# Optimization experiments

Measured on AMD Instinct MI355X. Metric: run time of the kernel, lower is better.

## Reference

```python
import jax, jax.numpy as jnp
import numpy as np
import math

S, B, H, NH = 2048, 2, 2048, 16
HN = H // NH  # 128, head dim


def _rope_cache(seq_len, hn):
    # inv_freqs over even indices, half_hn entries
    inv_freqs = 0.0001 ** (jnp.arange(0, hn, 2, dtype=jnp.float32) / hn)
    pos = jnp.arange(seq_len, dtype=jnp.float32)
    angles = pos[:, None] * inv_freqs  # [s, hn/2]
    return jnp.cos(angles), jnp.sin(angles)


def _apply_rope(x, cos, sin):
    # x: [s, b, np, hn]; cos/sin: [s, hn/2] broadcast over b, np
    half = x.shape[-1] // 2
    c = cos[:, None, None, :]
    s = sin[:, None, None, :]
    left, right = x[..., :half], x[..., half:]
    return jnp.concatenate((c * left - s * right, s * left + c * right), axis=-1)


def setup_inputs() -> dict:
    key = jax.random.key(0)
    k0, k1, k2 = jax.random.split(key, 3)
    hidden_states = jax.random.normal(k0, (S, B, H), dtype=jnp.float32)
    # causal additive mask, broadcast over batch and heads
    causal = jnp.tril(jnp.ones((S, S), dtype=bool))
    attention_mask = jnp.where(causal, 0.0, -1e9).astype(jnp.float32)[None, None]
    W_qkv = jax.random.normal(k1, (3 * H, H), dtype=jnp.float32) * 0.02
    b_qkv = jnp.zeros((3 * H,), dtype=jnp.float32)
    W_dense = jax.random.normal(k2, (H, H), dtype=jnp.float32) * 0.02
    b_dense = jnp.zeros((H,), dtype=jnp.float32)
    return {"hidden_states": hidden_states, "attention_mask": attention_mask,
            "W_qkv": W_qkv, "b_qkv": b_qkv, "W_dense": W_dense, "b_dense": b_dense}


def reference(hidden_states, attention_mask, W_qkv, b_qkv, W_dense, b_dense):
    s, b, h = hidden_states.shape
    # fused QKV projection: [s,b,3h] -> [s,b,np,3*hn] -> split per head
    mixed = hidden_states @ W_qkv.T + b_qkv
    mixed = mixed.reshape(s, b, NH, 3 * HN)
    q, k, v = jnp.split(mixed, 3, axis=-1)  # each [s,b,np,hn]
    cos, sin = _rope_cache(s, HN)
    q = _apply_rope(q, cos, sin)
    k = _apply_rope(k, cos, sin)
    norm_factor = math.sqrt(HN)  # coeff is None (scale_attn_by_inverse_layer_idx=False)
    scores = jnp.einsum('sbnh,tbnh->bnst', q, k) / norm_factor  # [b,np,sq,sk]
    scores = scores + attention_mask
    probs = jax.nn.softmax(scores, axis=-1)  # dropout p=0 in eval
    ctx = jnp.einsum('bnst,tbnh->sbnh', probs, v).reshape(s, b, h)
    return ctx @ W_dense.T + b_dense  # [s,b,h]
```

## Files before the change

kernel.cpp:

```cpp
#include <hip/hip_runtime.h>

#define SEQ   2048
#define BATCH 2
#define HID   2048
#define NHEAD 16
#define HDIM  128
#define MTOT  4096
#define KDIM  2048

typedef __attribute__((ext_vector_type(8))) short  bf16x8;
typedef __attribute__((ext_vector_type(4))) float  f32x4;
typedef __attribute__((ext_vector_type(4))) unsigned short u16x4;
typedef __attribute__((ext_vector_type(8))) unsigned short u16x8;

__device__ __forceinline__ unsigned short f2bf(float x) {
  unsigned u = __float_as_uint(x);
  u += 0x7fffu + ((u >> 16) & 1u);
  return (unsigned short)(u >> 16);
}

__device__ __forceinline__ float fexp2(float x) {
  float r;
  asm("v_exp_f32 %0, %1" : "=v"(r) : "v"(x));
  return r;
}

__device__ __forceinline__ void gl_lds16(const void* g, void* l) {
  __builtin_amdgcn_global_load_lds(
      (__attribute__((address_space(1))) void*)g,
      (__attribute__((address_space(3))) void*)l, 16, 0, 0);
}

__device__ __forceinline__ f32x4 mfma16(bf16x8 a, bf16x8 b, f32x4 c) {
  return __builtin_amdgcn_mfma_f32_16x16x32_bf16(a, b, c, 0, 0, 0);
}

__global__ __launch_bounds__(256, 8)
void conv_swz(const float* __restrict__ src, unsigned short* __restrict__ dst) {
  int i = blockIdx.x * 256 + threadIdx.x;
  int base = i << 2;
  int r = base >> 11, k = base & 2047;
  f32x4 v = *(const f32x4*)(src + base);
  int kp = k ^ (((r >> 1) & 3) << 3);
  u16x4 o;
  o[0] = f2bf(v[0]); o[1] = f2bf(v[1]); o[2] = f2bf(v[2]); o[3] = f2bf(v[3]);
  *(u16x4*)(dst + (size_t)r * 2048 + kp) = o;
}

__global__ __launch_bounds__(256, 8)
void rope_cache_k(float* __restrict__ cosT, float* __restrict__ sinT) {
  int idx = blockIdx.x * 256 + threadIdx.x;
  int s = idx >> 6, i = idx & 63;
  float inv = powf(1e-4f, (float)i * (1.0f / 64.0f));
  float a = (float)s * inv;
  cosT[idx] = cosf(a);
  sinT[idx] = sinf(a);
}

__global__ __launch_bounds__(512, 2)
void gemm_qkv(const unsigned short* __restrict__ A,
              const unsigned short* __restrict__ Bt,
              const float* __restrict__ bias,
              unsigned short* __restrict__ Qs,
              unsigned short* __restrict__ Ks,
              unsigned short* __restrict__ Vp,
              const float* __restrict__ cosT,
              const float* __restrict__ sinT)
{
  __shared__ alignas(16) char lds[98304];
  const int tid = threadIdx.x;
  const int wid = tid >> 6, lane = tid & 63, g = lane >> 4, c = lane & 15;
  const int wr = wid >> 2, wc = wid & 3;

  const int bid = blockIdx.x;
  const int swz = (bid & 7) * 64 + (bid >> 3);
  const int nblk = swz & 15, mblk = swz >> 4;
  const int m0 = mblk << 7;
  const int n0 = nblk * 384;
  const int nh = nblk;

  char* ldsb = (char*)lds;
  const int slotg = (g ^ ((c >> 1) & 3)) << 4;
  const char* ldsAr = ldsb + (wr * 64 + c) * 64 + slotg;
  const char* ldsBr = ldsb + 24576 + (wc * 16 + c) * 64 + slotg;

  const char* gA = (const char*)A  + (size_t)(m0 + (tid >> 2)) * 4096 + (tid & 3) * 16;
  const char* gB = (const char*)Bt + (size_t)(n0 + (tid >> 2)) * 4096 + (tid & 3) * 16;
  char* lA = ldsb + tid * 16;
  char* lB = ldsb + 24576 + tid * 16;

#define STG_A(T, BUF) gl_lds16(gA + (T) * 64, lA + (BUF) * 8192)
#define STG_B(T, BUF) do { const char* _g = gB + (T) * 64; char* _l = lB + (BUF) * 24576; \
    gl_lds16(_g, _l); gl_lds16(_g + 524288, _l + 8192); gl_lds16(_g + 1048576, _l + 16384); } while (0)

  f32x4 acc[4][6];
#pragma unroll
  for (int i = 0; i < 4; ++i)
#pragma unroll
    for (int j = 0; j < 6; ++j) {
      acc[i][j][0] = 0.f; acc[i][j][1] = 0.f; acc[i][j][2] = 0.f; acc[i][j][3] = 0.f;
    }

  bf16x8 a[4], b0[3], b1[3];
  const int NT = KDIM / 32;

#define PH0(BUF, STAGE) do {                                                \
    _Pragma("unroll")                                                       \
    for (int mf = 0; mf < 4; ++mf)                                          \
      a[mf] = *(const bf16x8*)(ldsAr + (BUF) * 8192 + mf * 1024);           \
    _Pragma("unroll")                                                       \
    for (int nl = 0; nl < 3; ++nl)                                          \
      b0[nl] = *(const bf16x8*)(ldsBr + (BUF) * 24576 + nl * 4096);         \
    STAGE;                                                                  \
    __builtin_amdgcn_s_barrier();                                           \
    asm volatile("s_waitcnt lgkmcnt(0)" ::: "memory");                      \
    __builtin_amdgcn_s_setprio(1);                                          \
    _Pragma("unroll")                                                       \
    for (int mf = 0; mf < 4; ++mf)                                          \
      _Pragma("unroll")                                                     \
      for (int nl = 0; nl < 3; ++nl)                                        \
        acc[mf][nl] = mfma16(a[mf], b0[nl], acc[mf][nl]);                   \
    __builtin_amdgcn_s_setprio(0);                                          \
    __builtin_amdgcn_s_barrier();                                           \
  } while (0)

#define PH1(BUF, STAGE, VMW) do {                                           \
    _Pragma("unroll")                                                       \
    for (int nl = 0; nl < 3; ++nl)                                          \
      b1[nl] = *(const bf16x8*)(ldsBr + (BUF) * 24576 + (nl + 3) * 4096);   \
    STAGE;                                                                  \
    __builtin_amdgcn_s_barrier();                                           \
    asm volatile("s_waitcnt lgkmcnt(0)" ::: "memory");                      \
    __builtin_amdgcn_s_setprio(1);                                          \
    _Pragma("unroll")                                                       \
    for (int mf = 0; mf < 4; ++mf)                                          \
      _Pragma("unroll")                                                     \
      for (int nl = 0; nl < 3; ++nl)                                        \
        acc[mf][nl + 3] = mfma16(a[mf], b1[nl], acc[mf][nl + 3]);           \
    __builtin_amdgcn_s_setprio(0);                                          \
    VMW;                                                                    \
    __builtin_amdgcn_s_barrier();                                           \
  } while (0)

#define TILE(T, BUF, BUF2) do {                                             \
    PH0(BUF, { if ((T) + 2 < NT) STG_A((T) + 2, BUF2); });                  \
    PH1(BUF, { if ((T) + 2 < NT) STG_B((T) + 2, BUF2); },                   \
       { if ((T) + 2 < NT) { asm volatile("s_waitcnt vmcnt(4)" ::: "memory"); } \
         else              { asm volatile("s_waitcnt vmcnt(0)" ::: "memory"); } }); \
  } while (0)

  STG_A(0, 0); STG_B(0, 0);
  STG_A(1, 1); STG_B(1, 1);
  asm volatile("s_waitcnt vmcnt(4)" ::: "memory");
  __builtin_amdgcn_s_barrier();

  for (int t = 0; t < 63; t += 3) {
    TILE(t, 0, 2);
    TILE(t + 1, 1, 0);
    TILE(t + 2, 2, 1);
  }
  TILE(63, 0, 2);

  const float qsc = 0.08838834764831845f * 1.4426950408889634f;
  const int dl = wc * 16 + c;
#pragma unroll
  for (int ar = 0; ar < 4; ++ar) {
#pragma unroll
    for (int rr = 0; rr < 4; ++rr) {
      int m = m0 + wr * 64 + ar * 16 + g * 4 + rr;
      int s = m >> 1, bb = m & 1;
      size_t plane = (size_t)(bb * NHEAD + nh) * (SEQ * HDIM);
      int swb = (s & 7) << 3;
      float co = cosT[s * 64 + dl], si = sinT[s * 64 + dl];
      {
        float xl = acc[ar][0][rr] + bias[n0 + dl];
        float xr = acc[ar][1][rr] + bias[n0 + 64 + dl];
        Qs[plane + (size_t)s * HDIM + (dl ^ swb)]        = f2bf((co * xl - si * xr) * qsc);
        Qs[plane + (size_t)s * HDIM + ((dl + 64) ^ swb)] = f2bf((si * xl + co * xr) * qsc);
      }
      {
        float xl = acc[ar][2][rr] + bias[n0 + 128 + dl];
        float xr = acc[ar][3][rr] + bias[n0 + 192 + dl];
        Ks[plane + (size_t)s * HDIM + (dl ^ swb)]        = f2bf(co * xl - si * xr);
        Ks[plane + (size_t)s * HDIM + ((dl + 64) ^ swb)] = f2bf(si * xl + co * xr);
      }
      Vp[plane + (size_t)s * HDIM + dl]      = f2bf(acc[ar][4][rr] + bias[n0 + 256 + dl]);
      Vp[plane + (size_t)s * HDIM + dl + 64] = f2bf(acc[ar][5][rr] + bias[n0 + 320 + dl]);
    }
  }
#undef TILE
#undef PH0
#undef PH1
#undef STG_A
#undef STG_B
}

__global__ __launch_bounds__(512, 2)
void gemm_out(const unsigned short* __restrict__ A,
              const unsigned short* __restrict__ Bt,
              const float* __restrict__ bias,
              float* __restrict__ Cout)
{
  __shared__ alignas(16) char lds[73728];
  const int tid = threadIdx.x;
  const int wid = tid >> 6, lane = tid & 63, g = lane >> 4, c = lane & 15;
  const int wr = wid >> 2, wc = wid & 3;

  const int bid = blockIdx.x;
  const int swz = (bid & 7) * 32 + (bid >> 3);
  const int nblk = swz >> 5, mblk = swz & 31;
  const int m0 = mblk << 7, n0 = nblk << 8;

  char* ldsb = (char*)lds;
  const int slotg = (g ^ ((c >> 1) & 3)) << 4;
  const char* ldsAr = ldsb + (wr * 64 + c) * 64 + slotg;
  const char* ldsBr = ldsb + 24576 + (wc * 64 + c) * 64 + slotg;

  const char* gA = (const char*)A  + (size_t)(m0 + (tid >> 2)) * 4096 + (tid & 3) * 16;
  const char* gB = (const char*)Bt + (size_t)(n0 + (tid >> 2)) * 4096 + (tid & 3) * 16;
  char* lA = ldsb + tid * 16;
  char* lB = ldsb + 24576 + tid * 16;

#define STG_A(T, BUF) gl_lds16(gA + (T) * 64, lA + (BUF) * 8192)
#define STG_B(T, BUF) do { const char* _g = gB + (T) * 64; char* _l = lB + (BUF) * 16384; \
    gl_lds16(_g, _l); gl_lds16(_g + 524288, _l + 8192); } while (0)

  f32x4 acc[4][4];
#pragma unroll
  for (int i = 0; i < 4; ++i)
#pragma unroll
    for (int j = 0; j < 4; ++j) {
      acc[i][j][0] = 0.f; acc[i][j][1] = 0.f; acc[i][j][2] = 0.f; acc[i][j][3] = 0.f;
    }

  bf16x8 a[4], b[4];
  const int NT = KDIM / 32;

#define TILE(T, BUF, BUF2) do {                                             \
    _Pragma("unroll")                                                       \
    for (int mf = 0; mf < 4; ++mf)                                          \
      a[mf] = *(const bf16x8*)(ldsAr + (BUF) * 8192 + mf * 1024);           \
    _Pragma("unroll")                                                       \
    for (int nl = 0; nl < 4; ++nl)                                          \
      b[nl] = *(const bf16x8*)(ldsBr + (BUF) * 16384 + nl * 1024);          \
    if ((T) + 2 < NT) { STG_A((T) + 2, BUF2); STG_B((T) + 2, BUF2); }       \
    __builtin_amdgcn_s_barrier();                                           \
    asm volatile("s_waitcnt lgkmcnt(0)" ::: "memory");                      \
    __builtin_amdgcn_s_setprio(1);                                          \
    _Pragma("unroll")                                                       \
    for (int mf = 0; mf < 4; ++mf)                                          \
      _Pragma("unroll")                                                     \
      for (int nl = 0; nl < 4; ++nl)                                        \
        acc[mf][nl] = mfma16(a[mf], b[nl], acc[mf][nl]);                    \
    __builtin_amdgcn_s_setprio(0);                                          \
    if ((T) + 2 < NT) { asm volatile("s_waitcnt vmcnt(3)" ::: "memory"); }  \
    else              { asm volatile("s_waitcnt vmcnt(0)" ::: "memory"); }  \
    __builtin_amdgcn_s_barrier();                                           \
  } while (0)

  STG_A(0, 0); STG_B(0, 0);
  STG_A(1, 1); STG_B(1, 1);
  asm volatile("s_waitcnt vmcnt(3)" ::: "memory");
  __builtin_amdgcn_s_barrier();

  for (int t = 0; t < 63; t += 3) {
    TILE(t, 0, 2);
    TILE(t + 1, 1, 0);
    TILE(t + 2, 2, 1);
  }
  TILE(63, 0, 2);

#pragma unroll
  for (int mf = 0; mf < 4; ++mf)
#pragma unroll
    for (int rr = 0; rr < 4; ++rr) {
      int m = m0 + wr * 64 + mf * 16 + g * 4 + rr;
#pragma unroll
      for (int nl = 0; nl < 4; ++nl) {
        int n = n0 + wc * 64 + nl * 16 + c;
        Cout[(size_t)m * HID + n] = acc[mf][nl][rr] + bias[n];
      }
    }
#undef TILE
#undef STG_A
#undef STG_B
}

__global__ __launch_bounds__(256, 4)
void transpose_v(const unsigned short* __restrict__ Vp, unsigned short* __restrict__ Vt) {
  __shared__ alignas(16) unsigned short T[64 * 136];
  const int plane = blockIdx.x >> 5;
  const int t0 = (blockIdx.x & 31) << 6;
  const size_t pbase = (size_t)plane * (SEQ * HDIM);
  const int tid = threadIdx.x;
  {
    int t = tid >> 2, d0 = (tid & 3) << 5;
    const unsigned short* src = Vp + pbase + (size_t)(t0 + t) * HDIM + d0;
#pragma unroll
    for (int j = 0; j < 4; ++j) {
      u16x8 v = *(const u16x8*)(src + j * 8);
      *(u16x8*)(&T[t * 136 + d0 + j * 8]) = v;
    }
  }
  __syncthreads();
  {
    int d = tid >> 1, half = tid & 1;
    unsigned short* dstp = Vt + pbase + (size_t)d * SEQ;
    int swb = (d & 7) << 3;
#pragma unroll
    for (int gg = 0; gg < 4; ++gg) {
      u16x8 v;
#pragma unroll
      for (int e = 0; e < 8; ++e)
        v[e] = T[(half * 32 + gg * 8 + e) * 136 + d];
      int tloc = half * 32 + gg * 8;
      *(u16x8*)(dstp + ((t0 + tloc) ^ swb)) = v;
    }
  }
}

__global__ __launch_bounds__(256, 2)
void attn(const unsigned short* __restrict__ Qs,
          const unsigned short* __restrict__ Ks,
          const unsigned short* __restrict__ Vt,
          unsigned short* __restrict__ ctx)
{
  __shared__ alignas(16) unsigned short Klds[2][64 * 128];
  __shared__ alignas(16) unsigned short Vlds[128 * 64];
  __shared__ alignas(16) unsigned short Plds[128 * 72];
  const int tid = threadIdx.x;
  const int w = tid >> 6, lane = tid & 63, g = lane >> 4, c = lane & 15;
  const int bid = blockIdx.x;
  const int head = bid & 31;
  const int qb = (bid < 256) ? (15 - (bid >> 5)) : ((bid >> 5) - 8);
  const int q0 = qb << 7;
  const size_t plane = (size_t)head * (SEQ * HDIM);
  const unsigned short* Qp = Qs + plane;
  const unsigned short* Kp = Ks + plane;
  const unsigned short* Vp = Vt + plane;

  bf16x8 qf[2][4];
#pragma unroll
  for (int q2 = 0; q2 < 2; ++q2) {
    int s = q0 + w * 32 + q2 * 16 + c;
    int swb = (s & 7) << 3;
#pragma unroll
    for (int kk = 0; kk < 4; ++kk) {
      int d0 = kk * 32 + g * 8;
      qf[q2][kk] = *(const bf16x8*)(Qp + (size_t)s * HDIM + (d0 ^ swb));
    }
  }

  f32x4 accO[2][8];
#pragma unroll
  for (int i = 0; i < 2; ++i)
#pragma unroll
    for (int j = 0; j < 8; ++j) {
      accO[i][j][0] = 0.f; accO[i][j][1] = 0.f; accO[i][j][2] = 0.f; accO[i][j][3] = 0.f;
    }
  float mrun[2] = { -1e30f, -1e30f };
  float lrun[2] = { 0.f, 0.f };

  const char* KgBase = (const char*)Kp + (tid >> 4) * 256 + (tid & 15) * 16;
  const char* VgBase = (const char*)Vp + (size_t)(tid >> 3) * 4096 + (tid & 7) * 16;
  char* VldsW = (char*)Vlds + w * 1024;

  const int ntiles = (q0 >> 6) + 2;
  const int qminw = q0 + w * 32;
  const int qmaxw = qminw + 31;

#pragma unroll
  for (int i = 0; i < 4; ++i)
    gl_lds16(KgBase, (char*)Klds[0] + w * 1024 + i * 4096), KgBase += 4096;
  KgBase -= 16384;

  for (int kt = 0; kt < ntiles; ++kt) {
    const int t0 = kt << 6;
    const bool havenext = (kt + 1 < ntiles);

#pragma unroll
    for (int i = 0; i < 4; ++i)
      gl_lds16(VgBase + t0 * 2 + (size_t)i * 131072, VldsW + i * 4096);
    if (havenext) {
      char* kdst = (char*)Klds[(kt + 1) & 1] + w * 1024;
#pragma unroll
      for (int i = 0; i < 4; ++i)
        gl_lds16(KgBase + (size_t)(t0 + 64) * 256 + i * 4096, kdst + i * 4096);
    }
    if (havenext) asm volatile("s_waitcnt vmcnt(8)" ::: "memory");
    else          asm volatile("s_waitcnt vmcnt(4)" ::: "memory");
    __builtin_amdgcn_s_barrier();

    if (t0 <= qmaxw) {
      const char* Kb = (const char*)Klds[kt & 1];
      f32x4 sacc[4][2];
#pragma unroll
      for (int i = 0; i < 4; ++i)
#pragma unroll
        for (int j = 0; j < 2; ++j) {
          sacc[i][j][0] = 0.f; sacc[i][j][1] = 0.f; sacc[i][j][2] = 0.f; sacc[i][j][3] = 0.f;
        }
      __builtin_amdgcn_s_setprio(1);
#pragma unroll
      for (int kk = 0; kk < 4; ++kk) {
        bf16x8 kf[4];
#pragma unroll
        for (int ta = 0; ta < 4; ++ta) {
          int t = ta * 16 + c;
          int d0 = kk * 32 + g * 8;
          kf[ta] = *(const bf16x8*)(Kb + t * 256 + ((d0 ^ ((t & 7) << 3)) << 1));
        }
#pragma unroll
        for (int ta = 0; ta < 4; ++ta)
#pragma unroll
          for (int q2 = 0; q2 < 2; ++q2)
            sacc[ta][q2] = mfma16(kf[ta], qf[q2][kk], sacc[ta][q2]);
      }
      __builtin_amdgcn_s_setprio(0);

      if (t0 + 63 > qminw) {
#pragma unroll
        for (int ta = 0; ta < 4; ++ta)
#pragma unroll
          for (int q2 = 0; q2 < 2; ++q2)
#pragma unroll
            for (int r = 0; r < 4; ++r) {
              int t = t0 + ta * 16 + g * 4 + r;
              int q = qminw + q2 * 16 + c;
              if (t > q) sacc[ta][q2][r] = -30000.f;
            }
      }

      float corr[2];
      bool resc = false;
#pragma unroll
      for (int q2 = 0; q2 < 2; ++q2) {
        float mx = -30000.f;
#pragma unroll
        for (int ta = 0; ta < 4; ++ta)
          mx = fmaxf(mx, fmaxf(fmaxf(sacc[ta][q2][0], sacc[ta][q2][1]),
                               fmaxf(sacc[ta][q2][2], sacc[ta][q2][3])));
        mx = fmaxf(mx, __shfl_xor(mx, 16));
        mx = fmaxf(mx, __shfl_xor(mx, 32));
        bool rs = mx > mrun[q2] + 8.0f;
        resc |= rs;
        float mnew = rs ? mx : mrun[q2];
        corr[q2] = fexp2(mrun[q2] - mnew);
        mrun[q2] = mnew;
        float ls = 0.f;
#pragma unroll
        for (int ta = 0; ta < 4; ++ta)
#pragma unroll
          for (int r = 0; r < 4; ++r) {
            float e = fexp2(sacc[ta][q2][r] - mnew);
            sacc[ta][q2][r] = e;
            ls += e;
          }
        ls += __shfl_xor(ls, 16);
        ls += __shfl_xor(ls, 32);
        lrun[q2] = lrun[q2] * corr[q2] + ls;
      }

      if (__any(resc)) {
#pragma unroll
        for (int q2 = 0; q2 < 2; ++q2)
#pragma unroll
          for (int r = 0; r < 4; ++r) {
            float cD = __shfl(corr[q2], (lane & 48) | (((lane >> 4) << 2) + r));
#pragma unroll
            for (int fn = 0; fn < 8; ++fn) accO[q2][fn][r] *= cD;
          }
      }

#pragma unroll
      for (int q2 = 0; q2 < 2; ++q2) {
        int prow = w * 32 + q2 * 16 + c;
#pragma unroll
        for (int ta = 0; ta < 4; ++ta) {
          u16x4 pk;
          pk[0] = f2bf(sacc[ta][q2][0]); pk[1] = f2bf(sacc[ta][q2][1]);
          pk[2] = f2bf(sacc[ta][q2][2]); pk[3] = f2bf(sacc[ta][q2][3]);
          *(u16x4*)(&Plds[prow * 72 + ta * 16 + g * 4]) = pk;
        }
      }
    }

    if (havenext) asm volatile("s_waitcnt vmcnt(4)" ::: "memory");
    else          asm volatile("s_waitcnt vmcnt(0)" ::: "memory");
    __builtin_amdgcn_s_barrier();

    if (t0 <= qmaxw) {
      __builtin_amdgcn_s_setprio(1);
#pragma unroll
      for (int kk = 0; kk < 2; ++kk) {
        bf16x8 pa[2];
#pragma unroll
        for (int q2 = 0; q2 < 2; ++q2)
          pa[q2] = *(const bf16x8*)((const char*)Plds + (w * 32 + q2 * 16 + c) * 144 + (kk * 32 + g * 8) * 2);
#pragma unroll
        for (int fn = 0; fn < 8; ++fn) {
          int d = fn * 16 + c;
          int tt = kk * 32 + g * 8;
          bf16x8 vb = *(const bf16x8*)((const char*)Vlds + d * 128 + ((tt ^ ((d & 7) << 3)) << 1));
#pragma unroll
          for (int q2 = 0; q2 < 2; ++q2)
            accO[q2][fn] = mfma16(pa[q2], vb, accO[q2][fn]);
        }
      }
      __builtin_amdgcn_s_setprio(0);
    }
    __builtin_amdgcn_s_barrier();
  }

  const int b = head >> 4, nh = head & 15;
  float linv[2] = { 1.0f / lrun[0], 1.0f / lrun[1] };
#pragma unroll
  for (int q2 = 0; q2 < 2; ++q2)
#pragma unroll
    for (int r = 0; r < 4; ++r) {
      float inv = __shfl(linv[q2], (lane & 48) | (((lane >> 4) << 2) + r));
      int q = q0 + w * 32 + q2 * 16 + g * 4 + r;
      int m = q * 2 + b;
      int swb = ((m >> 1) & 3) << 3;
#pragma unroll
      for (int fn = 0; fn < 8; ++fn) {
        int h = nh * 128 + fn * 16 + c;
        ctx[(size_t)m * HID + (h ^ swb)] = f2bf(accO[q2][fn][r] * inv);
      }
    }
}

extern "C" void kernel_launch(void* const* d_in, const int* in_sizes, int n_in,
                              void* d_out, int out_size, void* d_ws, size_t ws_size,
                              hipStream_t stream) {
  const float* hidden = (const float*)d_in[0];
  const float* Wqkv = (const float*)d_in[2];
  const float* bqkv = (const float*)d_in[3];
  const float* Wd   = (const float*)d_in[4];
  const float* bd   = (const float*)d_in[5];
  float* out = (float*)d_out;
  char* ws = (char*)d_ws;

  const size_t OFF_HID  = 0;
  const size_t OFF_WQKV = 16777216;
  const size_t OFF_WD   = 41943040;
  const size_t OFF_COS  = 50331648;
  const size_t OFF_SIN  = 50855936;
  const size_t OFF_Q    = 51380224;
  const size_t OFF_K    = 68157440;
  const size_t OFF_V    = 84934656;
  const size_t OFF_VT   = 101711872;
  if (ws_size < 118489088) return;

  unsigned short* hidb  = (unsigned short*)(ws + OFF_HID);
  unsigned short* wqkvb = (unsigned short*)(ws + OFF_WQKV);
  unsigned short* wdb   = (unsigned short*)(ws + OFF_WD);
  float* cosT = (float*)(ws + OFF_COS);
  float* sinT = (float*)(ws + OFF_SIN);
  unsigned short* Qsb = (unsigned short*)(ws + OFF_Q);
  unsigned short* Ksb = (unsigned short*)(ws + OFF_K);
  unsigned short* Vpb = (unsigned short*)(ws + OFF_V);
  unsigned short* Vtb = (unsigned short*)(ws + OFF_VT);
  unsigned short* ctxb = hidb;

  conv_swz<<<8192, 256, 0, stream>>>(hidden, hidb);
  conv_swz<<<12288, 256, 0, stream>>>(Wqkv, wqkvb);
  conv_swz<<<4096, 256, 0, stream>>>(Wd, wdb);
  rope_cache_k<<<512, 256, 0, stream>>>(cosT, sinT);

  gemm_qkv<<<512, 512, 0, stream>>>(hidb, wqkvb, bqkv, Qsb, Ksb, Vpb, cosT, sinT);
  transpose_v<<<1024, 256, 0, stream>>>(Vpb, Vtb);
  attn<<<512, 256, 0, stream>>>(Qsb, Ksb, Vtb, ctxb);
  gemm_out<<<256, 512, 0, stream>>>(ctxb, wdb, bd, out);
}
```

Before: 254.4 us.

## Merge prep kernels into one launch and simplify GEMM main-loop barriers

Folds the three fp32-to-bf16 conversion launches and the rope cache launch into a single prep kernel that picks its job by block index, removing three launch gaps. In both GEMMs the per-tile schedule is reworked: the next-tile global-to-LDS loads are issued first, the mid-tile barrier and explicit lgkmcnt wait are dropped, and the QKV kernel's two half-phases become one phase of 24 MFMAs. This cuts barrier count per K-step but relies on compiler-inserted LDS waits and gives up the finer interleave of loads with math.

Measured after the change: 249.4 us. No clear change (-2.0%).

```diff
diff --git a/kernel.cpp b/kernel.cpp
--- a/kernel.cpp
+++ b/kernel.cpp
@@ -36,25 +36,33 @@
 }
 
 __global__ __launch_bounds__(256, 8)
-void conv_swz(const float* __restrict__ src, unsigned short* __restrict__ dst) {
-  int i = blockIdx.x * 256 + threadIdx.x;
-  int base = i << 2;
-  int r = base >> 11, k = base & 2047;
-  f32x4 v = *(const f32x4*)(src + base);
-  int kp = k ^ (((r >> 1) & 3) << 3);
-  u16x4 o;
-  o[0] = f2bf(v[0]); o[1] = f2bf(v[1]); o[2] = f2bf(v[2]); o[3] = f2bf(v[3]);
-  *(u16x4*)(dst + (size_t)r * 2048 + kp) = o;
-}
-
-__global__ __launch_bounds__(256, 8)
-void rope_cache_k(float* __restrict__ cosT, float* __restrict__ sinT) {
-  int idx = blockIdx.x * 256 + threadIdx.x;
-  int s = idx >> 6, i = idx & 63;
-  float inv = powf(1e-4f, (float)i * (1.0f / 64.0f));
-  float a = (float)s * inv;
-  cosT[idx] = cosf(a);
-  sinT[idx] = sinf(a);
+void prep(const float* __restrict__ hidden, const float* __restrict__ Wqkv,
+          const float* __restrict__ Wd,
+          unsigned short* __restrict__ hidb, unsigned short* __restrict__ wqkvb,
+          unsigned short* __restrict__ wdb,
+          float* __restrict__ cosT, float* __restrict__ sinT) {
+  int bid = blockIdx.x;
+  if (bid < 24576) {
+    const float* src; unsigned short* dst; int lb;
+    if (bid < 8192)       { src = hidden; dst = hidb;  lb = bid; }
+    else if (bid < 20480) { src = Wqkv;   dst = wqkvb; lb = bid - 8192; }
+    else                  { src = Wd;     dst = wdb;   lb = bid - 20480; }
+    int i = lb * 256 + threadIdx.x;
+    int base = i << 2;
+    int r = base >> 11, k = base & 2047;
+    f32x4 v = *(const f32x4*)(src + base);
+    int kp = k ^ (((r >> 1) & 3) << 3);
+    u16x4 o;
+    o[0] = f2bf(v[0]); o[1] = f2bf(v[1]); o[2] = f2bf(v[2]); o[3] = f2bf(v[3]);
+    *(u16x4*)(dst + (size_t)r * 2048 + kp) = o;
+  } else {
+    int idx = (bid - 24576) * 256 + threadIdx.x;
+    int s = idx >> 6, i = idx & 63;
+    float inv = powf(1e-4f, (float)i * (1.0f / 64.0f));
+    float a = (float)s * inv;
+    cosT[idx] = cosf(a);
+    sinT[idx] = sinf(a);
+  }
 }
 
 __global__ __launch_bounds__(512, 2)
@@ -101,52 +109,27 @@
       acc[i][j][0] = 0.f; acc[i][j][1] = 0.f; acc[i][j][2] = 0.f; acc[i][j][3] = 0.f;
     }
 
-  bf16x8 a[4], b0[3], b1[3];
+  bf16x8 a[4], b[6];
   const int NT = KDIM / 32;
 
-#define PH0(BUF, STAGE) do {                                                \
+#define TILE(T, BUF, BUFN) do {                                             \
+    if ((T) + 2 < NT) { STG_A((T) + 2, BUFN); STG_B((T) + 2, BUFN); }       \
     _Pragma("unroll")                                                       \
     for (int mf = 0; mf < 4; ++mf)                                          \
       a[mf] = *(const bf16x8*)(ldsAr + (BUF) * 8192 + mf * 1024);           \
     _Pragma("unroll")                                                       \
-    for (int nl = 0; nl < 3; ++nl)                                          \
-      b0[nl] = *(const bf16x8*)(ldsBr + (BUF) * 24576 + nl * 4096);         \
-    STAGE;                                                                  \
-    __builtin_amdgcn_s_barrier();                                           \
-    asm volatile("s_waitcnt lgkmcnt(0)" ::: "memory");                      \
+    for (int nl = 0; nl < 6; ++nl)                                          \
+      b[nl] = *(const bf16x8*)(ldsBr + (BUF) * 24576 + nl * 4096);          \
     __builtin_amdgcn_s_setprio(1);                                          \
     _Pragma("unroll")                                                       \
     for (int mf = 0; mf < 4; ++mf)                                          \
       _Pragma("unroll")                                                     \
-      for (int nl = 0; nl < 3; ++nl)                                        \
-        acc[mf][nl] = mfma16(a[mf], b0[nl], acc[mf][nl]);                   \
+      for (int nl = 0; nl < 6; ++nl)                                        \
+        acc[mf][nl] = mfma16(a[mf], b[nl], acc[mf][nl]);                    \
     __builtin_amdgcn_s_setprio(0);                                          \
+    if ((T) + 2 < NT) { asm volatile("s_waitcnt vmcnt(4)" ::: "memory"); }  \
+    else              { asm volatile("s_waitcnt vmcnt(0)" ::: "memory"); }  \
     __builtin_amdgcn_s_barrier();                                           \
-  } while (0)
-
-#define PH1(BUF, STAGE, VMW) do {                                           \
-    _Pragma("unroll")                                                       \
-    for (int nl = 0; nl < 3; ++nl)                                          \
-      b1[nl] = *(const bf16x8*)(ldsBr + (BUF) * 24576 + (nl + 3) * 4096);   \
-    STAGE;                                                                  \
-    __builtin_amdgcn_s_barrier();                                           \
-    asm volatile("s_waitcnt lgkmcnt(0)" ::: "memory");                      \
-    __builtin_amdgcn_s_setprio(1);                                          \
-    _Pragma("unroll")                                                       \
-    for (int mf = 0; mf < 4; ++mf)                                          \
-      _Pragma("unroll")                                                     \
-      for (int nl = 0; nl < 3; ++nl)                                        \
-        acc[mf][nl + 3] = mfma16(a[mf], b1[nl], acc[mf][nl + 3]);           \
-    __builtin_amdgcn_s_setprio(0);                                          \
-    VMW;                                                                    \
-    __builtin_amdgcn_s_barrier();                                           \
-  } while (0)
-
-#define TILE(T, BUF, BUF2) do {                                             \
-    PH0(BUF, { if ((T) + 2 < NT) STG_A((T) + 2, BUF2); });                  \
-    PH1(BUF, { if ((T) + 2 < NT) STG_B((T) + 2, BUF2); },                   \
-       { if ((T) + 2 < NT) { asm volatile("s_waitcnt vmcnt(4)" ::: "memory"); } \
-         else              { asm volatile("s_waitcnt vmcnt(0)" ::: "memory"); } }); \
   } while (0)
 
   STG_A(0, 0); STG_B(0, 0);
@@ -189,8 +172,6 @@
     }
   }
 #undef TILE
-#undef PH0
-#undef PH1
 #undef STG_A
 #undef STG_B
 }
@@ -236,16 +217,14 @@
   bf16x8 a[4], b[4];
   const int NT = KDIM / 32;
 
-#define TILE(T, BUF, BUF2) do {                                             \
+#define TILE(T, BUF, BUFN) do {                                             \
+    if ((T) + 2 < NT) { STG_A((T) + 2, BUFN); STG_B((T) + 2, BUFN); }       \
     _Pragma("unroll")                                                       \
     for (int mf = 0; mf < 4; ++mf)                                          \
       a[mf] = *(const bf16x8*)(ldsAr + (BUF) * 8192 + mf * 1024);           \
     _Pragma("unroll")                                                       \
     for (int nl = 0; nl < 4; ++nl)                                          \
       b[nl] = *(const bf16x8*)(ldsBr + (BUF) * 16384 + nl * 1024);          \
-    if ((T) + 2 < NT) { STG_A((T) + 2, BUF2); STG_B((T) + 2, BUF2); }       \
-    __builtin_amdgcn_s_barrier();                                           \
-    asm volatile("s_waitcnt lgkmcnt(0)" ::: "memory");                      \
     __builtin_amdgcn_s_setprio(1);                                          \
     _Pragma("unroll")                                                       \
     for (int mf = 0; mf < 4; ++mf)                                          \
@@ -563,10 +542,7 @@
   unsigned short* Vtb = (unsigned short*)(ws + OFF_VT);
   unsigned short* ctxb = hidb;
 
-  conv_swz<<<8192, 256, 0, stream>>>(hidden, hidb);
-  conv_swz<<<12288, 256, 0, stream>>>(Wqkv, wqkvb);
-  conv_swz<<<4096, 256, 0, stream>>>(Wd, wdb);
-  rope_cache_k<<<512, 256, 0, stream>>>(cosT, sinT);
+  prep<<<25088, 256, 0, stream>>>(hidden, Wqkv, Wd, hidb, wqkvb, wdb, cosT, sinT);
 
   gemm_qkv<<<512, 512, 0, stream>>>(hidb, wqkvb, bqkv, Qsb, Ksb, Vpb, cosT, sinT);
   transpose_v<<<1024, 256, 0, stream>>>(Vpb, Vtb);
```
